# Performance work log

Measured on AMD Instinct MI355X. Metric: run time of the kernel, lower is better.

## Reference

```python
import jax, jax.numpy as jnp
import numpy as np

LR = 0.01  # init kwarg lr
N, D_IN, D_OUT = 64, 1024, 256


def _qf(A):
    # QR retraction with sign correction so diag(R) >= 0 (canonical Q).
    Q, R = jnp.linalg.qr(A)  # reduced: Q [n,Din,Dout], R [n,Dout,Dout]
    d = jnp.diagonal(R, axis1=-2, axis2=-1)
    sign = jnp.sign(jnp.sign(d) + 0.5)  # maps 0 -> +1
    return Q * sign[:, None, :]


def setup_inputs() -> dict:
    key = jax.random.key(0)
    k1, k2, k3, k4 = jax.random.split(key, 4)
    grad = jax.random.normal(k1, (N, D_IN, D_OUT), dtype=jnp.float32)
    # start M on the Stiefel manifold (columns orthonormal), as the optimizee assumes
    M = _qf(jax.random.normal(k2, (N, D_IN, D_OUT), dtype=jnp.float32))
    state = jnp.zeros((1,), dtype=jnp.float32)
    L_0 = jax.random.uniform(k3, (N, D_IN), dtype=jnp.float32) + 0.1
    R_0 = jax.random.uniform(k4, (N, D_OUT), dtype=jnp.float32) + 0.1
    return {"grad": grad, "M": M, "state": state, "L_0": L_0, "R_0": R_0}


def reference(grad, M, state, L_0, R_0):
    n, Din, Dout = M.shape
    # row/col second-moment accumulators (the per-sample torch loop, vectorized over n)
    g2_row = jnp.einsum('nio,nio->ni', grad, grad)  # diag(U U^T), [n, Din]
    g2_col = jnp.einsum('nio,nio->no', grad, grad)  # diag(U^T U), [n, Dout]
    l = 0.5 * L_0 + 0.5 * g2_row / Dout
    ll = jnp.maximum(L_0, l)
    r = 0.5 * R_0 + 0.5 * g2_col / Din
    rr = jnp.maximum(R_0, r)
    # diag(ll^-1/4) @ U @ diag(rr^-1/4) as broadcast scaling
    UU = grad * (ll ** (-0.25))[:, :, None] * (rr ** (-0.25))[:, None, :]
    # w = M M^T ; PP = UU - w @ UU  (project off the current subspace)
    w = jnp.einsum('nio,njo->nij', M, M)            # [n, Din, Din]
    PP = UU - jnp.einsum('nij,njo->nio', w, UU)
    update = PP * LR                                 # torch: update[i] = PP * self.lr
    # retraction called with update * lr (lr applied twice, faithful to source)
    M_new = _qf(M - update * LR)
    return (M_new, state, ll, rr)
```

## Files before the change

kernel.cpp:

```cpp
#include <hip/hip_runtime.h>

typedef unsigned short u16t;
typedef unsigned int   u32t;
typedef __bf16 bf16x8 __attribute__((ext_vector_type(8)));
typedef float  f32x4  __attribute__((ext_vector_type(4)));

#define NB   64
#define DIN  1024
#define DOUT 256
#define EPS  1e-4f
#define KP   68

#define OUT_STATE (NB*DIN*DOUT)
#define OUT_LL    (OUT_STATE + 1)
#define OUT_RR    (OUT_LL + NB*DIN)

__device__ __forceinline__ u16t f2b(float x) {
    u32t u = __builtin_bit_cast(u32t, x);
    u += 0x7FFFu + ((u >> 16) & 1u);
    return (u16t)(u >> 16);
}
__device__ __forceinline__ float b2f(u16t h) {
    return __builtin_bit_cast(float, ((u32t)h) << 16);
}
__device__ __forceinline__ bf16x8 ld_frag(const u16t* p) {
    uint2 lo = *(const uint2*)(p);
    uint2 hi = *(const uint2*)(p + 4);
    union { uint4 u; bf16x8 v; } x;
    x.u = make_uint4(lo.x, lo.y, hi.x, hi.y);
    return x.v;
}
__device__ __forceinline__ void st8(u16t* p, u32t a, u32t b) {
    *(uint2*)(p) = make_uint2(a, b);
}

__global__ __launch_bounds__(256) void k_prep(
    const float* __restrict__ grad, const float* __restrict__ L0,
    float* __restrict__ out, float* __restrict__ AS, float* __restrict__ CP)
{
    const int bid = blockIdx.x;
    const int n = bid & 63;
    const int chunk = bid >> 6;
    const int wave = threadIdx.x >> 6, lane = threadIdx.x & 63;
    const float* gb = grad + ((size_t)n << 18);

    float4 cacc = {0.f, 0.f, 0.f, 0.f};
    const int i0 = chunk * 32 + wave * 8;
    #pragma unroll
    for (int r = 0; r < 8; ++r) {
        const int i = i0 + r;
        const float4 v = *(const float4*)(gb + (size_t)i * 256 + lane * 4);
        float s = v.x*v.x + v.y*v.y + v.z*v.z + v.w*v.w;
        cacc.x += v.x*v.x; cacc.y += v.y*v.y; cacc.z += v.z*v.z; cacc.w += v.w*v.w;
        #pragma unroll
        for (int off = 32; off; off >>= 1) s += __shfl_xor(s, off);
        const float l0 = L0[n * DIN + i];
        const float ll = fmaxf(l0, 0.5f * l0 + s * (0.5f / DOUT));
        if (lane == 0) {
            out[OUT_LL + n * DIN + i] = ll;
            AS[n * DIN + i] = rsqrtf(sqrtf(ll));
        }
    }
    const int slot = chunk * 4 + wave;
    *(float4*)(CP + ((size_t)(n * 128 + slot)) * 256 + lane * 4) = cacc;
}

__global__ __launch_bounds__(256) void k_cols(
    const float* __restrict__ R0, const float* __restrict__ state,
    float* __restrict__ out, float* __restrict__ BS, const float* __restrict__ CP)
{
    const int n = blockIdx.x, o = threadIdx.x;
    const float* cp = CP + (size_t)n * 128 * 256 + o;
    float s = 0.f;
    #pragma unroll 8
    for (int k = 0; k < 128; ++k) s += cp[k * 256];
    const float r0 = R0[n * DOUT + o];
    const float rr = fmaxf(r0, 0.5f * r0 + s * (0.5f / DIN));
    out[OUT_RR + n * DOUT + o] = rr;
    BS[n * DOUT + o] = rsqrtf(sqrtf(rr));
    if (n == 0 && o == 0) out[OUT_STATE] = state[0];
}

__global__ __launch_bounds__(256, 4) void k_T(
    const float* __restrict__ grad, const float* __restrict__ M,
    const float* __restrict__ AS, const float* __restrict__ BS,
    u16t* __restrict__ TT)
{
    __shared__ u16t sA[128 * KP];
    __shared__ u16t sB[64 * KP];
    const int bid = blockIdx.x;
    const int n = bid & 63;
    const int tile = bid >> 6;
    const int o0 = (tile & 1) * 128, p0 = (tile >> 1) * 64;
    const int t = threadIdx.x, lane = t & 63, w = t >> 6;
    const int wr = w >> 1, wc = w & 1, t16 = lane & 15, g4 = lane >> 4;
    const float* Gn = grad + ((size_t)n << 18);
    const float* Mn = M + ((size_t)n << 18);
    const float* An = AS + n * DIN;
    f32x4 acc[4][2] = {};

    for (int ch = 0; ch < 16; ++ch) {
        const int ib = ch * 64;
        __syncthreads();
        #pragma unroll
        for (int r = 0; r < 16; ++r) {
            const int il = w * 16 + r;
            const int ig = ib + il;
            const float a = An[ig];
            const float* gsrc = Gn + (size_t)ig * 256 + o0;
            const float* msrc = Mn + (size_t)ig * 256 + p0;
            sA[(size_t)lane * KP + il]        = f2b(gsrc[lane] * a);
            sA[(size_t)(lane + 64) * KP + il] = f2b(gsrc[lane + 64] * a);
            sB[(size_t)lane * KP + il]        = f2b(msrc[lane]);
        }
        __syncthreads();
        #pragma unroll
        for (int kb = 0; kb < 2; ++kb) {
            const int ko = kb * 32 + g4 * 8;
            bf16x8 fa[4], fb[2];
            #pragma unroll
            for (int fm = 0; fm < 4; ++fm)
                fa[fm] = ld_frag(sA + (wr*64 + fm*16 + t16) * KP + ko);
            #pragma unroll
            for (int fn = 0; fn < 2; ++fn)
                fb[fn] = ld_frag(sB + (wc*32 + fn*16 + t16) * KP + ko);
            #pragma unroll
            for (int fm = 0; fm < 4; ++fm)
                #pragma unroll
                for (int fn = 0; fn < 2; ++fn)
                    acc[fm][fn] = __builtin_amdgcn_mfma_f32_16x16x32_bf16(fa[fm], fb[fn], acc[fm][fn], 0, 0, 0);
        }
    }
    const float* bs = BS + n * DOUT;
    u16t* TTn = TT + ((size_t)n << 16);
    #pragma unroll
    for (int fm = 0; fm < 4; ++fm)
        #pragma unroll
        for (int fn = 0; fn < 2; ++fn) {
            const int p = p0 + wc*32 + fn*16 + t16;
            #pragma unroll
            for (int r = 0; r < 4; ++r) {
                const int o = o0 + wr*64 + fm*16 + g4*4 + r;
                TTn[o * 256 + p] = f2b(acc[fm][fn][r] * bs[o]);
            }
        }
}

__global__ __launch_bounds__(256, 3) void k_fuse(
    const float* __restrict__ M, const float* __restrict__ grad,
    const float* __restrict__ BS, const u16t* __restrict__ TT,
    float* __restrict__ out)
{
    __shared__ u16t sA[128 * KP];
    __shared__ u16t sB[128 * KP];
    __shared__ float sa_[128];
    const int bid = blockIdx.x;
    const int n = bid & 63;
    const int tile = bid >> 6;
    const int i0 = (tile & 7) * 128, o0 = (tile >> 3) * 128;
    const int t = threadIdx.x, lane = t & 63, w = t >> 6;
    const int wr = w >> 1, wc = w & 1, t16 = lane & 15, g4 = lane >> 4;
    const float* Mn = M + ((size_t)n << 18);
    const float* Gr = grad + ((size_t)n << 18);
    const u16t* TTn = TT + ((size_t)n << 16);
    if (t < 128) {
        const float ll = out[OUT_LL + n * DIN + i0 + t];
        sa_[t] = rsqrtf(sqrtf(ll));
    }
    float4 rMa[8];
    uint4  rTb[4];
    f32x4 acc[4][4] = {};

#define FU_LOAD(ch) { const int pb_ = (ch) * 64; \
    _Pragma("unroll") for (int j = 0; j < 8; ++j) { \
        const int s = j * 256 + t, row = s >> 4, c4 = (s & 15) * 4; \
        rMa[j] = *(const float4*)(Mn + (size_t)(i0 + row) * 256 + pb_ + c4); } \
    _Pragma("unroll") for (int j = 0; j < 4; ++j) { \
        const int s = j * 256 + t, row = s >> 3, c8 = (s & 7) * 8; \
        rTb[j] = *(const uint4*)(TTn + (size_t)(o0 + row) * 256 + pb_ + c8); } }

    FU_LOAD(0);
    for (int ch = 0; ch < 4; ++ch) {
        __syncthreads();
        #pragma unroll
        for (int j = 0; j < 8; ++j) {
            const int s = j * 256 + t, row = s >> 4, c4 = (s & 15) * 4;
            const float4 v = rMa[j];
            ushort4 h = { f2b(v.x), f2b(v.y), f2b(v.z), f2b(v.w) };
            *(ushort4*)(sA + row * KP + c4) = h;
        }
        #pragma unroll
        for (int j = 0; j < 4; ++j) {
            const int s = j * 256 + t, row = s >> 3, c8 = (s & 7) * 8;
            st8(sB + row * KP + c8,     rTb[j].x, rTb[j].y);
            st8(sB + row * KP + c8 + 4, rTb[j].z, rTb[j].w);
        }
        __syncthreads();
        if (ch < 3) FU_LOAD(ch + 1);
        #pragma unroll
        for (int kb = 0; kb < 2; ++kb) {
            const int ko = kb * 32 + g4 * 8;
            bf16x8 fa[4], fb[4];
            #pragma unroll
            for (int fm = 0; fm < 4; ++fm)
                fa[fm] = ld_frag(sA + (wr*64 + fm*16 + t16) * KP + ko);
            #pragma unroll
            for (int fn = 0; fn < 4; ++fn)
                fb[fn] = ld_frag(sB + (wc*64 + fn*16 + t16) * KP + ko);
            #pragma unroll
            for (int fm = 0; fm < 4; ++fm)
                #pragma unroll
                for (int fn = 0; fn < 4; ++fn)
                    acc[fm][fn] = __builtin_amdgcn_mfma_f32_16x16x32_bf16(fa[fm], fb[fn], acc[fm][fn], 0, 0, 0);
        }
    }
    const float* bs = BS + n * DOUT;
    float* outn = out + ((size_t)n << 18);
    #pragma unroll
    for (int fm = 0; fm < 4; ++fm)
        #pragma unroll
        for (int fn = 0; fn < 4; ++fn) {
            const int o = o0 + wc*64 + fn*16 + t16;
            const float bo = bs[o];
            #pragma unroll
            for (int r = 0; r < 4; ++r) {
                const int il = wr*64 + fm*16 + g4*4 + r;
                const int i = i0 + il;
                const size_t idx = (size_t)i * 256 + o;
                outn[idx] = Mn[idx] + EPS * (acc[fm][fn][r] - bo * sa_[il] * Gr[idx]);
            }
        }
}

extern "C" void kernel_launch(void* const* d_in, const int* in_sizes, int n_in,
                              void* d_out, int out_size, void* d_ws, size_t ws_size,
                              hipStream_t stream) {
    const float* grad  = (const float*)d_in[0];
    const float* M     = (const float*)d_in[1];
    const float* state = (const float*)d_in[2];
    const float* L0    = (const float*)d_in[3];
    const float* R0    = (const float*)d_in[4];
    float* out = (float*)d_out;
    char* wsb = (char*)d_ws;

    u16t*  TT = (u16t*)(wsb);
    float* CP = (float*)(wsb + ((size_t)8 << 20));
    float* AS = (float*)(wsb + ((size_t)16 << 20));
    float* BS = (float*)(wsb + ((size_t)17 << 20));

    k_prep <<<2048, 256, 0, stream>>>(grad, L0, out, AS, CP);
    k_cols <<<64,   256, 0, stream>>>(R0, state, out, BS, CP);
    k_T    <<<512,  256, 0, stream>>>(grad, M, AS, BS, TT);
    k_fuse <<<1024, 256, 0, stream>>>(M, grad, BS, TT, out);
}
```

Baseline: 102.9 us.

## Split-K the T GEMM into four partials with a separate reduction kernel

The k_T GEMM (grad^T scaled times M over the 1024-long inner dimension) is split into four K-quarters, so the launch grows from 512 to 2048 blocks and more of the GPU stays busy. Each quarter writes bf16 partial results to a new workspace buffer, and a new k_red kernel sums them and applies the column scale. The LDS staging stores are also packed two bf16 values per 32-bit write. This adds a kernel launch and extra partial-sum traffic, and it rounds each partial to bf16 before summing, which costs some accuracy.

```diff
diff --git a/kernel.cpp b/kernel.cpp
--- a/kernel.cpp
+++ b/kernel.cpp
@@ -22,6 +22,9 @@
 }
 __device__ __forceinline__ float b2f(u16t h) {
     return __builtin_bit_cast(float, ((u32t)h) << 16);
+}
+__device__ __forceinline__ u32t pk(u16t lo, u16t hi) {
+    return (u32t)lo | ((u32t)hi << 16);
 }
 __device__ __forceinline__ bf16x8 ld_frag(const u16t* p) {
     uint2 lo = *(const uint2*)(p);
@@ -83,14 +86,14 @@
 
 __global__ __launch_bounds__(256, 4) void k_T(
     const float* __restrict__ grad, const float* __restrict__ M,
-    const float* __restrict__ AS, const float* __restrict__ BS,
-    u16t* __restrict__ TT)
+    const float* __restrict__ AS, u16t* __restrict__ TTP)
 {
     __shared__ u16t sA[128 * KP];
     __shared__ u16t sB[64 * KP];
     const int bid = blockIdx.x;
     const int n = bid & 63;
-    const int tile = bid >> 6;
+    const int tile = (bid >> 6) & 7;
+    const int kq = bid >> 9;
     const int o0 = (tile & 1) * 128, p0 = (tile >> 1) * 64;
     const int t = threadIdx.x, lane = t & 63, w = t >> 6;
     const int wr = w >> 1, wc = w & 1, t16 = lane & 15, g4 = lane >> 4;
@@ -99,19 +102,24 @@
     const float* An = AS + n * DIN;
     f32x4 acc[4][2] = {};
 
-    for (int ch = 0; ch < 16; ++ch) {
-        const int ib = ch * 64;
-        __syncthreads();
-        #pragma unroll
-        for (int r = 0; r < 16; ++r) {
-            const int il = w * 16 + r;
-            const int ig = ib + il;
-            const float a = An[ig];
-            const float* gsrc = Gn + (size_t)ig * 256 + o0;
-            const float* msrc = Mn + (size_t)ig * 256 + p0;
-            sA[(size_t)lane * KP + il]        = f2b(gsrc[lane] * a);
-            sA[(size_t)(lane + 64) * KP + il] = f2b(gsrc[lane + 64] * a);
-            sB[(size_t)lane * KP + il]        = f2b(msrc[lane]);
+    for (int ch = 0; ch < 4; ++ch) {
+        const int ib = kq * 256 + ch * 64;
+        __syncthreads();
+        #pragma unroll
+        for (int r = 0; r < 8; ++r) {
+            const int il0 = w * 16 + 2 * r;
+            const int ig0 = ib + il0;
+            const float a0 = An[ig0], a1 = An[ig0 + 1];
+            const float* g0 = Gn + (size_t)ig0 * 256 + o0;
+            const float* g1 = g0 + 256;
+            const float* m0 = Mn + (size_t)ig0 * 256 + p0;
+            const float* m1 = m0 + 256;
+            *(u32t*)&sA[(size_t)lane * KP + il0] =
+                pk(f2b(g0[lane] * a0),      f2b(g1[lane] * a1));
+            *(u32t*)&sA[(size_t)(lane + 64) * KP + il0] =
+                pk(f2b(g0[lane + 64] * a0), f2b(g1[lane + 64] * a1));
+            *(u32t*)&sB[(size_t)lane * KP + il0] =
+                pk(f2b(m0[lane]),           f2b(m1[lane]));
         }
         __syncthreads();
         #pragma unroll
@@ -131,8 +139,7 @@
                     acc[fm][fn] = __builtin_amdgcn_mfma_f32_16x16x32_bf16(fa[fm], fb[fn], acc[fm][fn], 0, 0, 0);
         }
     }
-    const float* bs = BS + n * DOUT;
-    u16t* TTn = TT + ((size_t)n << 16);
+    u16t* TTq = TTP + ((size_t)kq << 22) + ((size_t)n << 16);
     #pragma unroll
     for (int fm = 0; fm < 4; ++fm)
         #pragma unroll
@@ -141,9 +148,33 @@
             #pragma unroll
             for (int r = 0; r < 4; ++r) {
                 const int o = o0 + wr*64 + fm*16 + g4*4 + r;
-                TTn[o * 256 + p] = f2b(acc[fm][fn][r] * bs[o]);
+                TTq[o * 256 + p] = f2b(acc[fm][fn][r]);
             }
         }
+}
+
+__global__ __launch_bounds__(256) void k_red(
+    const u16t* __restrict__ TTP, const float* __restrict__ BS,
+    u16t* __restrict__ TT)
+{
+    const size_t idx8 = ((size_t)blockIdx.x * 256 + threadIdx.x) * 8;
+    const int n = (int)(idx8 >> 16);
+    const int o = (int)((idx8 >> 8) & 255);
+    const float bo = BS[n * DOUT + o];
+    uint4 v0 = *(const uint4*)(TTP + ((size_t)0 << 22) + idx8);
+    uint4 v1 = *(const uint4*)(TTP + ((size_t)1 << 22) + idx8);
+    uint4 v2 = *(const uint4*)(TTP + ((size_t)2 << 22) + idx8);
+    uint4 v3 = *(const uint4*)(TTP + ((size_t)3 << 22) + idx8);
+    const u16t* a = (const u16t*)&v0;
+    const u16t* b = (const u16t*)&v1;
+    const u16t* c = (const u16t*)&v2;
+    const u16t* d = (const u16t*)&v3;
+    u16t r[8];
+    #pragma unroll
+    for (int e = 0; e < 8; ++e)
+        r[e] = f2b((b2f(a[e]) + b2f(b[e]) + b2f(c[e]) + b2f(d[e])) * bo);
+    const u32t* rw = (const u32t*)r;
+    *(uint4*)(TT + idx8) = make_uint4(rw[0], rw[1], rw[2], rw[3]);
 }
 
 __global__ __launch_bounds__(256, 3) void k_fuse(
@@ -243,13 +274,15 @@
     float* out = (float*)d_out;
     char* wsb = (char*)d_ws;
 
-    u16t*  TT = (u16t*)(wsb);
-    float* CP = (float*)(wsb + ((size_t)8 << 20));
-    float* AS = (float*)(wsb + ((size_t)16 << 20));
-    float* BS = (float*)(wsb + ((size_t)17 << 20));
+    u16t*  TT  = (u16t*)(wsb);
+    u16t*  TTP = (u16t*)(wsb + ((size_t)8 << 20));
+    float* CP  = (float*)(wsb + ((size_t)40 << 20));
+    float* AS  = (float*)(wsb + ((size_t)48 << 20));
+    float* BS  = (float*)(wsb + ((size_t)49 << 20));
 
     k_prep <<<2048, 256, 0, stream>>>(grad, L0, out, AS, CP);
     k_cols <<<64,   256, 0, stream>>>(R0, state, out, BS, CP);
-    k_T    <<<512,  256, 0, stream>>>(grad, M, AS, BS, TT);
+    k_T    <<<2048, 256, 0, stream>>>(grad, M, AS, TTP);
+    k_red  <<<2048, 256, 0, stream>>>(TTP, BS, TT);
     k_fuse <<<1024, 256, 0, stream>>>(M, grad, BS, TT, out);
 }
```

Measured after the change: 110.1 us. 1.07x slower.
